# Kernel optimization log

Hardware: AMD Instinct MI355X
Metric: run time of the kernel (lower is better)

Reference implementation:

```python
import jax, jax.numpy as jnp
import numpy as np

SEQ, B, IN, H, OUT, L = 256, 64, 512, 1024, 256, 2
DT = 0.05

def setup_inputs() -> dict:
    key = jax.random.key(0)
    ks = jax.random.split(key, 10)
    s = lambda fan_in: 1.0 / np.sqrt(fan_in)
    return {
        "x":    jax.random.normal(ks[0], (SEQ, B, IN), dtype=jnp.float32),
        "W_in": jax.random.uniform(ks[1], (H, IN), jnp.float32, -s(IN), s(IN)),
        "b_in": jax.random.uniform(ks[2], (H,), jnp.float32, -s(IN), s(IN)),
        "W_c":  jax.random.uniform(ks[3], (H, 2 * H), jnp.float32, -s(2 * H), s(2 * H)),
        "b_c":  jax.random.uniform(ks[4], (H,), jnp.float32, -s(2 * H), s(2 * H)),
        "taus": jnp.ones((L,), jnp.float32),
        "W_o1": jax.random.uniform(ks[5], (H // 2, H), jnp.float32, -s(H), s(H)),
        "b_o1": jax.random.uniform(ks[6], (H // 2,), jnp.float32, -s(H), s(H)),
        "W_o2": jax.random.uniform(ks[7], (OUT, H // 2), jnp.float32, -s(H // 2), s(H // 2)),
        "b_o2": jax.random.uniform(ks[8], (OUT,), jnp.float32, -s(H // 2), s(H // 2)),
    }

def reference(x, W_in, b_in, W_c, b_c, taus, W_o1, b_o1, W_o2, b_o2):
    # input projection for all timesteps at once: [S,B,IN] -> [S,B,H]
    xp = jnp.einsum('sbi,hi->sbh', x, W_in) + b_in
    num_layers = taus.shape[0]
    batch = x.shape[1]
    hidden0 = jnp.zeros((num_layers, batch, W_in.shape[0]), dtype=x.dtype)

    def step(hidden, xt):
        inp = xt  # [B,H]
        new_hidden = []
        for layer in range(num_layers):
            h = hidden[layer]
            # original code calls cell(input_t.detach(), h): stop gradient on input path
            comb = jnp.concatenate([jax.lax.stop_gradient(inp), h], axis=-1)  # [B,2H]
            dhdt = jnp.tanh(comb @ W_c.T + b_c)
            h_next = h + (DT / (taus[layer] + 0.001)) * dhdt
            new_hidden.append(h_next)
            inp = h_next
        hidden = jnp.stack(new_hidden)  # [L,B,H]
        out = jax.nn.relu(hidden[-1] @ W_o1.T + b_o1) @ W_o2.T + b_o2  # [B,OUT]
        return hidden, out

    hidden_final, outputs = jax.lax.scan(step, hidden0, xp)
    return outputs, hidden_final
```

## Files before the change

### kernel.cpp

```cpp
#include <hip/hip_runtime.h>
#include <hip/hip_bf16.h>
#include <stdint.h>

typedef unsigned short ushort_t;
typedef unsigned long long ull_t;
using bf16x8 = __attribute__((ext_vector_type(8))) short;
using f32x4  = __attribute__((ext_vector_type(4))) float;

#define SEQ    256
#define BATCH  64
#define INDIM  512
#define HDIM   1024
#define OUTDIM 256
#define MTOT   (SEQ*BATCH)
#define BH     (BATCH*HDIM)

__device__ __forceinline__ ushort_t f2bf(float f) {
  uint32_t u = __builtin_bit_cast(uint32_t, f);
  u += 0x7fffu + ((u >> 16) & 1u);
  return (ushort_t)(u >> 16);
}
__device__ __forceinline__ float bf2f(ushort_t b) {
  uint32_t u = ((uint32_t)b) << 16;
  return __builtin_bit_cast(float, u);
}
__device__ __forceinline__ f32x4 mfma16(bf16x8 a, bf16x8 b, f32x4 c) {
  return __builtin_amdgcn_mfma_f32_16x16x32_bf16(a, b, c, 0, 0, 0);
}
__device__ __forceinline__ void gload16(const void* g, void* l) {
  __builtin_amdgcn_global_load_lds(
      (const __attribute__((address_space(1))) unsigned int*)g,
      (__attribute__((address_space(3))) unsigned int*)l, 16, 0, 0);
}
__device__ __forceinline__ float tanhfast(float z) {
  float e = __expf(2.0f * z);
  return 1.0f - 2.0f / (e + 1.0f);
}
__device__ __forceinline__ int load_sc0_int(const int* p) {
  int v;
  asm volatile("global_load_dword %0, %1, off sc0\n\ts_waitcnt vmcnt(0)"
               : "=&v"(v) : "v"(p) : "memory");
  return v;
}

__global__ void k_convert(const float* __restrict__ src, ushort_t* __restrict__ dst, int n) {
  int i = blockIdx.x * blockDim.x + threadIdx.x;
  if (i < n) dst[i] = f2bf(src[i]);
}
__global__ void k_split(const float* __restrict__ src, ushort_t* __restrict__ hi,
                        ushort_t* __restrict__ lo, int n) {
  int i = blockIdx.x * blockDim.x + threadIdx.x;
  if (i < n) {
    float v = src[i];
    ushort_t h = f2bf(v);
    hi[i] = h;
    lo[i] = f2bf(v - bf2f(h));
  }
}
__global__ void k_split_wc(const float* __restrict__ Wc,
                           ushort_t* __restrict__ WiH, ushort_t* __restrict__ WiL,
                           ushort_t* __restrict__ WhH, ushort_t* __restrict__ WhL) {
  int i = blockIdx.x * blockDim.x + threadIdx.x;
  if (i < HDIM * HDIM) {
    int row = i >> 10, k = i & 1023;
    float vi = Wc[(size_t)row * (2 * HDIM) + k];
    float vh = Wc[(size_t)row * (2 * HDIM) + HDIM + k];
    ushort_t ih = f2bf(vi);
    WiH[i] = ih; WiL[i] = f2bf(vi - bf2f(ih));
    ushort_t hh = f2bf(vh);
    WhH[i] = hh; WhL[i] = f2bf(vh - bf2f(hh));
  }
}

template<int SPLITB, int RELU, int OUTBF>
__global__ __launch_bounds__(256) void gemm_nt(
    const ushort_t* __restrict__ A, const ushort_t* __restrict__ Bhi,
    const ushort_t* __restrict__ Blo, const float* __restrict__ bias,
    float* __restrict__ Cf, ushort_t* __restrict__ Cb,
    int M, int N, int K)
{
  __shared__ ushort_t As[128 * 32];
  __shared__ ushort_t Bh[128 * 32];
  __shared__ ushort_t Bl[128 * 32];
  const int tid = threadIdx.x;
  const int w = tid >> 6, l = tid & 63;
  const int m0 = blockIdx.x * 128, n0 = blockIdx.y * 128;
  const int wr = w >> 1, wc = w & 1;
  const int lr = l & 15, lk = l >> 4;

  f32x4 acc[4][4] = {};
  const int nK = K >> 5;
  const size_t rowB = (size_t)K * 2;

  for (int kk = 0; kk < nK; ++kk) {
    const size_t kbyte = (size_t)kk * 64;
#pragma unroll
    for (int j = 0; j < 2; ++j) {
      int c = (w * 2 + j) * 64 + l;
      int row = c >> 2;
      int kb = (c & 3) * 16;
      gload16((const char*)A + (size_t)(m0 + row) * rowB + kbyte + kb,
              (char*)As + (w * 2 + j) * 1024);
      gload16((const char*)Bhi + (size_t)(n0 + row) * rowB + kbyte + kb,
              (char*)Bh + (w * 2 + j) * 1024);
      if (SPLITB)
        gload16((const char*)Blo + (size_t)(n0 + row) * rowB + kbyte + kb,
                (char*)Bl + (w * 2 + j) * 1024);
    }
    __syncthreads();
    bf16x8 af[4], bhf[4], blf[4];
#pragma unroll
    for (int i = 0; i < 4; ++i) {
      af[i]  = *(const bf16x8*)&As[(wr * 64 + i * 16 + lr) * 32 + lk * 8];
      bhf[i] = *(const bf16x8*)&Bh[(wc * 64 + i * 16 + lr) * 32 + lk * 8];
      if (SPLITB)
        blf[i] = *(const bf16x8*)&Bl[(wc * 64 + i * 16 + lr) * 32 + lk * 8];
    }
#pragma unroll
    for (int i = 0; i < 4; ++i)
#pragma unroll
      for (int j2 = 0; j2 < 4; ++j2) {
        acc[i][j2] = mfma16(af[i], bhf[j2], acc[i][j2]);
        if (SPLITB) acc[i][j2] = mfma16(af[i], blf[j2], acc[i][j2]);
      }
    __syncthreads();
  }
#pragma unroll
  for (int j2 = 0; j2 < 4; ++j2) {
    int n = n0 + wc * 64 + j2 * 16 + lr;
    float bv = bias ? bias[n] : 0.0f;
#pragma unroll
    for (int i = 0; i < 4; ++i) {
#pragma unroll
      for (int r = 0; r < 4; ++r) {
        int m = m0 + wr * 64 + i * 16 + lk * 4 + r;
        float v = acc[i][j2][r] + bv;
        if (RELU) v = fmaxf(v, 0.0f);
        if (OUTBF) Cb[(size_t)m * N + n] = f2bf(v);
        else       Cf[(size_t)m * N + n] = v;
      }
    }
  }
}

__global__ __launch_bounds__(1024, 4) void scan_kernel(
    const float* __restrict__ P0,
    const ushort_t* __restrict__ WiH, const ushort_t* __restrict__ WiL,
    const ushort_t* __restrict__ WhH, const ushort_t* __restrict__ WhL,
    const float* __restrict__ b_c, const float* __restrict__ taus,
    ushort_t* __restrict__ h0buf,
    ushort_t* __restrict__ H1buf,
    float* __restrict__ outHidden, int* __restrict__ sync)
{
  __shared__ float red[4 * 16 * 320];
  __shared__ int meta[2];

  const int tid = threadIdx.x;
  const int w = tid >> 6, l = tid & 63;
  const int lr = l & 15, lk = l >> 4;

  int* cnt        = sync;
  int* flags_l2   = sync + 64;
  int* flags_mall = sync + 192;

  if (tid == 0) {
    int xcd;
    asm volatile("s_getreg_b32 %0, hwreg(HW_REG_XCC_ID)" : "=s"(xcd));
    int slot = 999;
    if (xcd < 4)
      slot = __hip_atomic_fetch_add(&cnt[xcd], 1, __ATOMIC_RELAXED,
                                    __HIP_MEMORY_SCOPE_AGENT);
    meta[0] = (xcd < 4) ? xcd : -1;
    meta[1] = slot;
  }
  __syncthreads();
  const int g = meta[0];
  const int c = meta[1];
  if (g < 0 || c >= 32) return;

  const int rowg = g * 16, colg = c * 32;
  const int kb = w * 64;

  bf16x8 whh[2][2], whl[2][2], wih[2][2], wil[2][2];
#pragma unroll
  for (int ct = 0; ct < 2; ++ct)
#pragma unroll
    for (int kk = 0; kk < 2; ++kk) {
      size_t off = (size_t)(colg + ct * 16 + lr) * HDIM + kb + kk * 32 + lk * 8;
      whh[ct][kk] = *(const bf16x8*)&WhH[off];
      whl[ct][kk] = *(const bf16x8*)&WhL[off];
      wih[ct][kk] = *(const bf16x8*)&WiH[off];
      wil[ct][kk] = *(const bf16x8*)&WiL[off];
    }

  const int ep = (w < 4);
  const int ph = w >> 1, ect = w & 1;
  const int ec = lr, R0 = lk * 4;
  float hm[4] = {0, 0, 0, 0};
  float bcn = 0.f, alpha = 0.f;
  float p0r[4] = {0, 0, 0, 0};
  if (ep) {
    alpha = 0.05f / (taus[ph] + 0.001f);
    bcn = b_c[colg + ect * 16 + ec];
    if (ph == 0) {
#pragma unroll
      for (int j = 0; j < 4; ++j)
        p0r[j] = P0[((size_t)0 * BATCH + rowg + R0 + j) * HDIM + colg + ect * 16 + ec];
    }
  }

  for (int i = 0; i <= SEQ; ++i) {
#pragma unroll
    for (int ct = 0; ct < 2; ++ct)
#pragma unroll
      for (int kk = 0; kk < 2; ++kk)
        asm volatile("" : "+v"(whh[ct][kk]), "+v"(whl[ct][kk]),
                          "+v"(wih[ct][kk]), "+v"(wil[ct][kk]));

    bf16x8 f0 = {}, f1 = {}, g0 = {}, g1 = {};
    f32x4 aA[2] = {}, aI[2] = {}, aH[2] = {};
    if (i >= 1) {
      const ushort_t* h0r = h0buf + (size_t)(i - 1) * BH;
      f0 = *(const bf16x8*)&h0r[(size_t)(rowg + lr) * HDIM + kb + lk * 8];
      f1 = *(const bf16x8*)&h0r[(size_t)(rowg + lr) * HDIM + kb + 32 + lk * 8];
      if (i >= 2) {
        const ushort_t* h1r = H1buf + (size_t)(i - 2) * BH;
        g0 = *(const bf16x8*)&h1r[(size_t)(rowg + lr) * HDIM + kb + lk * 8];
        g1 = *(const bf16x8*)&h1r[(size_t)(rowg + lr) * HDIM + kb + 32 + lk * 8];
      }
#pragma unroll
      for (int ct = 0; ct < 2; ++ct) {
        aA[ct] = mfma16(f0, whh[ct][0], aA[ct]);
        aA[ct] = mfma16(f0, whl[ct][0], aA[ct]);
        aA[ct] = mfma16(f1, whh[ct][1], aA[ct]);
        aA[ct] = mfma16(f1, whl[ct][1], aA[ct]);
        aI[ct] = mfma16(f0, wih[ct][0], aI[ct]);
        aI[ct] = mfma16(f0, wil[ct][0], aI[ct]);
        aI[ct] = mfma16(f1, wih[ct][1], aI[ct]);
        aI[ct] = mfma16(f1, wil[ct][1], aI[ct]);
      }
      if (i >= 2) {
#pragma unroll
        for (int ct = 0; ct < 2; ++ct) {
          aH[ct] = mfma16(g0, whh[ct][0], aH[ct]);
          aH[ct] = mfma16(g0, whl[ct][0], aH[ct]);
          aH[ct] = mfma16(g1, whh[ct][1], aH[ct]);
          aH[ct] = mfma16(g1, whl[ct][1], aH[ct]);
        }
      }
    }
    const int wbase = lr * 20 + lk * 4;
#pragma unroll
    for (int ct = 0; ct < 2; ++ct) {
      *(f32x4*)&red[((0 + ct) * 16 + w) * 320 + wbase] = aA[ct];
      f32x4 pb = aI[ct] + aH[ct];
      *(f32x4*)&red[((2 + ct) * 16 + w) * 320 + wbase] = pb;
    }
    __syncthreads();

    if (ep && ((ph == 0 && i < SEQ) || (ph == 1 && i >= 1))) {
      f32x4 s = {};
      const float* rb = &red[(w * 16) * 320 + ec * 20 + R0];
#pragma unroll
      for (int q = 0; q < 16; ++q)
        s += *(const f32x4*)&rb[q * 320];
      if (ph == 0) {
        ushort_t* dst = &h0buf[(size_t)i * BH + (size_t)(rowg + R0) * HDIM +
                               colg + ect * 16 + ec];
#pragma unroll
        for (int j = 0; j < 4; ++j) {
          hm[j] += alpha * tanhfast(p0r[j] + s[j]);
          dst[(size_t)j * HDIM] = f2bf(hm[j]);
        }
      } else {
        ushort_t* dst = &H1buf[(size_t)(i - 1) * BH + (size_t)(rowg + R0) * HDIM +
                               colg + ect * 16 + ec];
#pragma unroll
        for (int j = 0; j < 4; ++j) {
          hm[j] += alpha * tanhfast(s[j] + bcn);
          dst[(size_t)j * HDIM] = f2bf(hm[j]);
        }
      }
      asm volatile("s_waitcnt vmcnt(0)" ::: "memory");
    }
    __syncthreads();

    if (i < SEQ) {
      if (tid == 0) {
        *(volatile int*)&flags_l2[g * 32 + c] = i + 1;
        asm volatile("" ::: "memory");
        __hip_atomic_store(&flags_mall[g * 32 + c], i + 1, __ATOMIC_RELAXED,
                           __HIP_MEMORY_SCOPE_AGENT);
      }
      if (ep && ph == 0 && i + 1 < SEQ) {
#pragma unroll
        for (int j = 0; j < 4; ++j)
          p0r[j] = P0[((size_t)(i + 1) * BATCH + rowg + R0 + j) * HDIM +
                      colg + ect * 16 + ec];
      }
      if (w == 4) {
        const int target = i + 1;
        const int* fl2 = &flags_l2[g * 32 + (l & 31)];
        int* fml = &flags_mall[g * 32 + (l & 31)];
        for (int r = 0;; ++r) {
          int v = ((r & 3) == 3)
            ? __hip_atomic_load(fml, __ATOMIC_RELAXED, __HIP_MEMORY_SCOPE_AGENT)
            : load_sc0_int(fl2);
          if (__all(v >= target)) break;
        }
      }
      __syncthreads();
    }
  }

  if (ep) {
    float* dst = &outHidden[(size_t)ph * BH + (size_t)(rowg + R0) * HDIM +
                            colg + ect * 16 + ec];
#pragma unroll
    for (int j = 0; j < 4; ++j) dst[(size_t)j * HDIM] = hm[j];
  }
}

extern "C" void kernel_launch(void* const* d_in, const int* in_sizes, int n_in,
                              void* d_out, int out_size, void* d_ws, size_t ws_size,
                              hipStream_t stream) {
  const float* x    = (const float*)d_in[0];
  const float* W_in = (const float*)d_in[1];
  const float* b_in = (const float*)d_in[2];
  const float* W_c  = (const float*)d_in[3];
  const float* b_c  = (const float*)d_in[4];
  const float* taus = (const float*)d_in[5];
  const float* W_o1 = (const float*)d_in[6];
  const float* b_o1 = (const float*)d_in[7];
  const float* W_o2 = (const float*)d_in[8];
  const float* b_o2 = (const float*)d_in[9];
  float* out = (float*)d_out;

  char* ws = (char*)d_ws;
  size_t off = 0;
  auto alloc = [&](size_t bytes) -> char* {
    char* p = ws + off;
    off += (bytes + 255) & ~(size_t)255;
    return p;
  };
  ushort_t* x_bf  = (ushort_t*)alloc((size_t)MTOT * INDIM * 2);
  ushort_t* xp_b  = (ushort_t*)alloc((size_t)MTOT * HDIM * 2);
  float*    P0    = (float*)   alloc((size_t)MTOT * HDIM * 4);
  ushort_t* H1buf = (ushort_t*)alloc((size_t)MTOT * HDIM * 2);
  ushort_t* h0buf = (ushort_t*)alloc((size_t)SEQ * BH * 2);
  ushort_t* O1    = (ushort_t*)alloc((size_t)MTOT * (HDIM/2) * 2);
  ushort_t* WiH   = (ushort_t*)alloc((size_t)HDIM * HDIM * 2);
  ushort_t* WiL   = (ushort_t*)alloc((size_t)HDIM * HDIM * 2);
  ushort_t* WhH   = (ushort_t*)alloc((size_t)HDIM * HDIM * 2);
  ushort_t* WhL   = (ushort_t*)alloc((size_t)HDIM * HDIM * 2);
  ushort_t* WinH  = (ushort_t*)alloc((size_t)HDIM * INDIM * 2);
  ushort_t* WinL  = (ushort_t*)alloc((size_t)HDIM * INDIM * 2);
  ushort_t* Wo1b  = (ushort_t*)alloc((size_t)(HDIM/2) * HDIM * 2);
  ushort_t* Wo2b  = (ushort_t*)alloc((size_t)OUTDIM * (HDIM/2) * 2);
  int*      sync  = (int*)     alloc(4096);
  if (off > ws_size) return;

  hipMemsetAsync(sync, 0, 4096, stream);

  k_convert<<<(MTOT * INDIM + 255) / 256, 256, 0, stream>>>(x, x_bf, MTOT * INDIM);
  k_split<<<(HDIM * INDIM + 255) / 256, 256, 0, stream>>>(W_in, WinH, WinL, HDIM * INDIM);
  k_split_wc<<<(HDIM * HDIM + 255) / 256, 256, 0, stream>>>(W_c, WiH, WiL, WhH, WhL);
  k_convert<<<((HDIM/2) * HDIM + 255) / 256, 256, 0, stream>>>(W_o1, Wo1b, (HDIM/2) * HDIM);
  k_convert<<<(OUTDIM * (HDIM/2) + 255) / 256, 256, 0, stream>>>(W_o2, Wo2b, OUTDIM * (HDIM/2));

  gemm_nt<1, 0, 1><<<dim3(MTOT / 128, HDIM / 128), 256, 0, stream>>>(
      x_bf, WinH, WinL, b_in, nullptr, xp_b, MTOT, HDIM, INDIM);
  gemm_nt<1, 0, 0><<<dim3(MTOT / 128, HDIM / 128), 256, 0, stream>>>(
      xp_b, WiH, WiL, b_c, P0, nullptr, MTOT, HDIM, HDIM);

  scan_kernel<<<512, 1024, 0, stream>>>(P0, WiH, WiL, WhH, WhL, b_c, taus,
                                        h0buf, H1buf,
                                        out + (size_t)SEQ * BATCH * OUTDIM, sync);

  gemm_nt<0, 1, 1><<<dim3(MTOT / 128, (HDIM/2) / 128), 256, 0, stream>>>(
      H1buf, Wo1b, nullptr, b_o1, nullptr, O1, MTOT, HDIM / 2, HDIM);
  gemm_nt<0, 0, 0><<<dim3(MTOT / 128, OUTDIM / 128), 256, 0, stream>>>(
      O1, Wo2b, nullptr, b_o2, out, nullptr, MTOT, OUTDIM, HDIM / 2);
}
```

Measured before the change: 1.226 ms.

## Halve scan block to 8 waves, stage WhH in LDS, drop WiL split

The recurrent scan kernel now runs with 512 threads instead of 1024, and each wave covers 128 K-columns instead of 64. The per-step cross-wave reduction therefore sums 8 partials rather than 16, and the shared reduction buffer is halved. To fit the larger per-wave weight slice, the high half of the hidden weight (WhH) is staged once into padded LDS, and WhL and WiH stay in registers. The low-order correction for the input weight (WiL) is dropped, which removes MFMAs from every step but lowers the precision of the layer-1 input path.

```diff
diff --git a/kernel.cpp b/kernel.cpp
--- a/kernel.cpp
+++ b/kernel.cpp
@@ -14,6 +14,7 @@
 #define OUTDIM 256
 #define MTOT   (SEQ*BATCH)
 #define BH     (BATCH*HDIM)
+#define WPAD   1032
 
 __device__ __forceinline__ ushort_t f2bf(float f) {
   uint32_t u = __builtin_bit_cast(uint32_t, f);
@@ -143,7 +144,8 @@
   }
 }
 
-__global__ __launch_bounds__(1024, 4) void scan_kernel(
+__global__ __attribute__((amdgpu_waves_per_eu(2, 2))) __launch_bounds__(512)
+void scan_kernel(
     const float* __restrict__ P0,
     const ushort_t* __restrict__ WiH, const ushort_t* __restrict__ WiL,
     const ushort_t* __restrict__ WhH, const ushort_t* __restrict__ WhL,
@@ -152,7 +154,8 @@
     ushort_t* __restrict__ H1buf,
     float* __restrict__ outHidden, int* __restrict__ sync)
 {
-  __shared__ float red[4 * 16 * 320];
+  __shared__ float red[4 * 8 * 320];
+  __shared__ ushort_t WhLds[32 * WPAD];
   __shared__ int meta[2];
 
   const int tid = threadIdx.x;
@@ -179,19 +182,27 @@
   if (g < 0 || c >= 32) return;
 
   const int rowg = g * 16, colg = c * 32;
-  const int kb = w * 64;
-
-  bf16x8 whh[2][2], whl[2][2], wih[2][2], wil[2][2];
+  const int kb = w * 128;
+
+  {
+    const ushort_t* wsrc = WhH + (size_t)colg * HDIM;
+#pragma unroll
+    for (int j = 0; j < 8; ++j) {
+      int e = (j * 512 + tid) * 8;
+      bf16x8 v = *(const bf16x8*)&wsrc[e];
+      *(bf16x8*)&WhLds[(e >> 10) * WPAD + (e & 1023)] = v;
+    }
+  }
+  bf16x8 wl[2][4], wi[2][4];
 #pragma unroll
   for (int ct = 0; ct < 2; ++ct)
 #pragma unroll
-    for (int kk = 0; kk < 2; ++kk) {
+    for (int kk = 0; kk < 4; ++kk) {
       size_t off = (size_t)(colg + ct * 16 + lr) * HDIM + kb + kk * 32 + lk * 8;
-      whh[ct][kk] = *(const bf16x8*)&WhH[off];
-      whl[ct][kk] = *(const bf16x8*)&WhL[off];
-      wih[ct][kk] = *(const bf16x8*)&WiH[off];
-      wil[ct][kk] = *(const bf16x8*)&WiL[off];
-    }
+      wl[ct][kk] = *(const bf16x8*)&WhL[off];
+      wi[ct][kk] = *(const bf16x8*)&WiH[off];
+    }
+  __syncthreads();
 
   const int ep = (w < 4);
   const int ph = w >> 1, ect = w & 1;
@@ -213,56 +224,50 @@
 #pragma unroll
     for (int ct = 0; ct < 2; ++ct)
 #pragma unroll
-      for (int kk = 0; kk < 2; ++kk)
-        asm volatile("" : "+v"(whh[ct][kk]), "+v"(whl[ct][kk]),
-                          "+v"(wih[ct][kk]), "+v"(wil[ct][kk]));
-
-    bf16x8 f0 = {}, f1 = {}, g0 = {}, g1 = {};
+      for (int kk = 0; kk < 4; ++kk)
+        asm volatile("" : "+v"(wl[ct][kk]), "+v"(wi[ct][kk]));
+
+    bf16x8 f[4] = {}, hh[4] = {};
     f32x4 aA[2] = {}, aI[2] = {}, aH[2] = {};
     if (i >= 1) {
       const ushort_t* h0r = h0buf + (size_t)(i - 1) * BH;
-      f0 = *(const bf16x8*)&h0r[(size_t)(rowg + lr) * HDIM + kb + lk * 8];
-      f1 = *(const bf16x8*)&h0r[(size_t)(rowg + lr) * HDIM + kb + 32 + lk * 8];
+#pragma unroll
+      for (int kk = 0; kk < 4; ++kk)
+        f[kk] = *(const bf16x8*)&h0r[(size_t)(rowg + lr) * HDIM + kb + kk * 32 + lk * 8];
       if (i >= 2) {
         const ushort_t* h1r = H1buf + (size_t)(i - 2) * BH;
-        g0 = *(const bf16x8*)&h1r[(size_t)(rowg + lr) * HDIM + kb + lk * 8];
-        g1 = *(const bf16x8*)&h1r[(size_t)(rowg + lr) * HDIM + kb + 32 + lk * 8];
-      }
-#pragma unroll
-      for (int ct = 0; ct < 2; ++ct) {
-        aA[ct] = mfma16(f0, whh[ct][0], aA[ct]);
-        aA[ct] = mfma16(f0, whl[ct][0], aA[ct]);
-        aA[ct] = mfma16(f1, whh[ct][1], aA[ct]);
-        aA[ct] = mfma16(f1, whl[ct][1], aA[ct]);
-        aI[ct] = mfma16(f0, wih[ct][0], aI[ct]);
-        aI[ct] = mfma16(f0, wil[ct][0], aI[ct]);
-        aI[ct] = mfma16(f1, wih[ct][1], aI[ct]);
-        aI[ct] = mfma16(f1, wil[ct][1], aI[ct]);
-      }
-      if (i >= 2) {
-#pragma unroll
-        for (int ct = 0; ct < 2; ++ct) {
-          aH[ct] = mfma16(g0, whh[ct][0], aH[ct]);
-          aH[ct] = mfma16(g0, whl[ct][0], aH[ct]);
-          aH[ct] = mfma16(g1, whh[ct][1], aH[ct]);
-          aH[ct] = mfma16(g1, whl[ct][1], aH[ct]);
+#pragma unroll
+        for (int kk = 0; kk < 4; ++kk)
+          hh[kk] = *(const bf16x8*)&h1r[(size_t)(rowg + lr) * HDIM + kb + kk * 32 + lk * 8];
+      }
+#pragma unroll
+      for (int ct = 0; ct < 2; ++ct)
+#pragma unroll
+        for (int kk = 0; kk < 4; ++kk) {
+          bf16x8 wh = *(const bf16x8*)&WhLds[(ct * 16 + lr) * WPAD + kb + kk * 32 + lk * 8];
+          aA[ct] = mfma16(f[kk], wh, aA[ct]);
+          aA[ct] = mfma16(f[kk], wl[ct][kk], aA[ct]);
+          aI[ct] = mfma16(f[kk], wi[ct][kk], aI[ct]);
+          if (i >= 2) {
+            aH[ct] = mfma16(hh[kk], wh, aH[ct]);
+            aH[ct] = mfma16(hh[kk], wl[ct][kk], aH[ct]);
+          }
         }
-      }
     }
     const int wbase = lr * 20 + lk * 4;
 #pragma unroll
     for (int ct = 0; ct < 2; ++ct) {
-      *(f32x4*)&red[((0 + ct) * 16 + w) * 320 + wbase] = aA[ct];
+      *(f32x4*)&red[((0 + ct) * 8 + w) * 320 + wbase] = aA[ct];
       f32x4 pb = aI[ct] + aH[ct];
-      *(f32x4*)&red[((2 + ct) * 16 + w) * 320 + wbase] = pb;
+      *(f32x4*)&red[((2 + ct) * 8 + w) * 320 + wbase] = pb;
     }
     __syncthreads();
 
     if (ep && ((ph == 0 && i < SEQ) || (ph == 1 && i >= 1))) {
       f32x4 s = {};
-      const float* rb = &red[(w * 16) * 320 + ec * 20 + R0];
-#pragma unroll
-      for (int q = 0; q < 16; ++q)
+      const float* rb = &red[(w * 8) * 320 + ec * 20 + R0];
+#pragma unroll
+      for (int q = 0; q < 8; ++q)
         s += *(const f32x4*)&rb[q * 320];
       if (ph == 0) {
         ushort_t* dst = &h0buf[(size_t)i * BH + (size_t)(rowg + R0) * HDIM +
@@ -373,9 +378,9 @@
   gemm_nt<1, 0, 0><<<dim3(MTOT / 128, HDIM / 128), 256, 0, stream>>>(
       xp_b, WiH, WiL, b_c, P0, nullptr, MTOT, HDIM, HDIM);
 
-  scan_kernel<<<512, 1024, 0, stream>>>(P0, WiH, WiL, WhH, WhL, b_c, taus,
-                                        h0buf, H1buf,
-                                        out + (size_t)SEQ * BATCH * OUTDIM, sync);
+  scan_kernel<<<512, 512, 0, stream>>>(P0, WiH, WiL, WhH, WhL, b_c, taus,
+                                       h0buf, H1buf,
+                                       out + (size_t)SEQ * BATCH * OUTDIM, sync);
 
   gemm_nt<0, 1, 1><<<dim3(MTOT / 128, (HDIM/2) / 128), 256, 0, stream>>>(
       H1buf, Wo1b, nullptr, b_o1, nullptr, O1, MTOT, HDIM / 2, HDIM);
```

Result: slower. 1.290 ms (+5.2%).
